# Performance work log

Hardware: AMD Instinct MI355X
Metric: run time of the kernel (lower is better)

The kernel has to match this reference:

```python
import jax, jax.numpy as jnp
import numpy as np

N, E, IN, H = 20000, 50000, 32, 64


def _lin_init(k, fan_in, shape):
    b = 1.0 / np.sqrt(fan_in)
    return jax.random.uniform(k, shape, jnp.float32, -b, b)


def setup_inputs() -> dict:
    key = jax.random.key(0)
    ks = jax.random.split(key, 16)
    inp = {
        "x": jax.random.normal(ks[0], (N, IN), jnp.float32),
        "edge_index": jax.random.randint(ks[1], (2, E), 0, N, dtype=jnp.int32),
        "edge_attr": jax.random.normal(ks[2], (E, 1, 2), jnp.float32),
        # layer 0: edge MLP 2->H->IN*H, root [IN,H], bias [H]
        "w1_0": _lin_init(ks[3], 2, (2, H)),
        "b1_0": _lin_init(ks[4], 2, (H,)),
        "w2_0": _lin_init(ks[5], H, (H, IN * H)),
        "b2_0": _lin_init(ks[6], H, (IN * H,)),
        "root_0": _lin_init(ks[7], IN, (IN, H)),
        "bias_0": _lin_init(ks[8], IN, (H,)),
        # layer 1: edge MLP 2->H->H*H, root [H,H], bias [H]
        "w1_1": _lin_init(ks[9], 2, (2, H)),
        "b1_1": _lin_init(ks[10], 2, (H,)),
        "w2_1": _lin_init(ks[11], H, (H, H * H)),
        "b2_1": _lin_init(ks[12], H, (H * H,)),
        "root_1": _lin_init(ks[13], H, (H, H)),
        "bias_1": _lin_init(ks[14], H, (H,)),
    }
    return inp


def _nnconv(x, src, dst, ea, w1, b1, w2, b2, root, bias, in_c, out_c):
    # per-edge weight matrices from edge-attr MLP: [E, in_c*out_c]
    h = jax.nn.relu(ea @ w1 + b1) @ w2 + b2
    W = h.reshape(-1, in_c, out_c)                     # [E, in, out]
    msg = jnp.einsum('ei,eio->eo', x[src], W)          # gather + per-edge matmul
    agg = jax.ops.segment_sum(msg, dst, num_segments=x.shape[0])  # scatter-add
    return agg + x @ root + bias                       # add aggr (PyG NNConv, aggr='add')


def reference(x, edge_index, edge_attr,
              w1_0, b1_0, w2_0, b2_0, root_0, bias_0,
              w1_1, b1_1, w2_1, b2_1, root_1, bias_1):
    src, dst = edge_index[0], edge_index[1]
    ea = edge_attr.reshape(edge_attr.shape[0], 2)      # [E, 2]
    x = jax.nn.relu(_nnconv(x, src, dst, ea, w1_0, b1_0, w2_0, b2_0, root_0, bias_0, IN, H))
    x = jax.nn.relu(_nnconv(x, src, dst, ea, w1_1, b1_1, w2_1, b2_1, root_1, bias_1, H, H))
    return x
```

## Files before the change

kernel.cpp:

```cpp
#include <hip/hip_runtime.h>

typedef _Float16 v8h __attribute__((ext_vector_type(8)));
typedef float v16f __attribute__((ext_vector_type(16)));

__global__ void prep_fused(const float* __restrict__ w2_0, const float* __restrict__ b2_0,
                           _Float16* __restrict__ BF0,
                           const float* __restrict__ w2_1, const float* __restrict__ b2_1,
                           _Float16* __restrict__ BF1,
                           const float* __restrict__ x, const float* __restrict__ root,
                           const float* __restrict__ bias, float* __restrict__ agg,
                           _Float16* __restrict__ xb, int N) {
    int idx = blockIdx.x * 256 + threadIdx.x;
    const int n0 = 264 * 512;
    const int n1 = 528 * 512;
    if (idx < n0 + n1) {
        const float* w2; const float* b2; _Float16* BF; int IN, rel;
        if (idx < n0) { w2 = w2_0; b2 = b2_0; BF = BF0; IN = 32; rel = idx; }
        else          { w2 = w2_1; b2 = b2_1; BF = BF1; IN = 64; rel = idx - n0; }
        int j = rel & 7, lane = (rel >> 3) & 63, f = rel >> 9;
        int nf = f & 1, kk16 = f >> 1;
        int ln = lane & 31, g2 = lane >> 5;
        int k = kk16 * 16 + g2 * 8 + j;
        int ko = k / IN, i = k - ko * IN;
        int o = nf * 32 + ln;
        float v = (ko < 64) ? w2[ko * (IN * 64) + i * 64 + o]
                : (ko == 64 ? b2[i * 64 + o] : 0.f);
        BF[rel] = (_Float16)v;
        return;
    }
    idx -= (n0 + n1);
    if (idx >= N * 64) return;
    int n = idx >> 6, o = idx & 63;
    float s = bias[o];
    const float* xr = x + (size_t)n * 32;
    #pragma unroll 8
    for (int i = 0; i < 32; ++i) s += xr[i] * root[i * 64 + o];
    agg[idx] = s;
    if (o < 32) xb[n * 32 + o] = (_Float16)xr[o];
}

__global__ void mid_kernel(const float* __restrict__ agg0, const float* __restrict__ root1,
                           const float* __restrict__ bias1, _Float16* __restrict__ x1b,
                           float* __restrict__ agg1, int N) {
    int idx = blockIdx.x * 256 + threadIdx.x;
    if (idx >= N * 64) return;
    int n = idx >> 6, o = idx & 63;
    const float* ar = agg0 + (size_t)n * 64;
    float s = bias1[o];
    #pragma unroll 8
    for (int i = 0; i < 64; ++i) s += fmaxf(ar[i], 0.f) * root1[i * 64 + o];
    agg1[idx] = s;
    x1b[idx] = (_Float16)fmaxf(agg0[idx], 0.f);
}

__global__ void final_relu(const float* __restrict__ agg1, float* __restrict__ out, int n) {
    int idx = blockIdx.x * 256 + threadIdx.x;
    if (idx < n) out[idx] = fmaxf(agg1[idx], 0.f);
}

template<int IN_C>
__global__ __launch_bounds__(256, 2)
void edge_gemm(const float* __restrict__ ea,
               const float* __restrict__ w1, const float* __restrict__ b1,
               const _Float16* __restrict__ xb, const _Float16* __restrict__ BF,
               const int* __restrict__ srcI, const int* __restrict__ dstI,
               float* __restrict__ agg, int E) {
    constexpr int PH  = IN_C / 16;
    constexpr int CPR = IN_C / 8;

    __shared__ __align__(16) _Float16 sh_x[128][IN_C];
    __shared__ _Float16 sh_r1[128][66];
    __shared__ float buf[128][65];
    __shared__ int sh_dst[128];

    int tid = threadIdx.x;
    int ebase = blockIdx.x * 128;
    int valid = E - ebase; if (valid > 128) valid = 128;

    if (tid < 128) {
        sh_dst[tid] = (tid < valid) ? dstI[ebase + tid] : 0;
        sh_r1[tid][64] = (_Float16)1.f;
        sh_r1[tid][65] = (_Float16)0.f;
    }
    for (int i = tid; i < 128 * 64; i += 256) {
        int e = i >> 6, j = i & 63;
        int ge = (e < valid) ? (ebase + e) : ebase;
        float a0 = ea[ge * 2], a1 = ea[ge * 2 + 1];
        sh_r1[e][j] = (_Float16)fmaxf(a0 * w1[j] + a1 * w1[64 + j] + b1[j], 0.f);
    }
    for (int i = tid; i < 128 * CPR; i += 256) {
        int r = i / CPR, c = i - r * CPR;
        int sidx = (r < valid) ? srcI[ebase + r] : 0;
        *(uint4*)&sh_x[r][c * 8] = *(const uint4*)(xb + (size_t)sidx * IN_C + (size_t)c * 8);
    }
    __syncthreads();

    int wv = tid >> 6, lane = tid & 63, ln = lane & 31, g2 = lane >> 5;
    int nf = wv & 1, kh = wv >> 1;

    v8h xs0[PH], xs1[PH], xs2[PH], xs3[PH];
    #pragma unroll
    for (int p = 0; p < PH; ++p) {
        xs0[p] = *(const v8h*)&sh_x[ln     ][p * 16 + g2 * 8];
        xs1[p] = *(const v8h*)&sh_x[ln + 32][p * 16 + g2 * 8];
        xs2[p] = *(const v8h*)&sh_x[ln + 64][p * 16 + g2 * 8];
        xs3[p] = *(const v8h*)&sh_x[ln + 96][p * 16 + g2 * 8];
    }

    v16f acc0 = {0,0,0,0,0,0,0,0,0,0,0,0,0,0,0,0};
    v16f acc1 = acc0, acc2 = acc0, acc3 = acc0;

    const uint4* bp = (const uint4*)BF + (size_t)nf * 64 + lane;
    int kb = kh * 33;

    uint4 b[PH], bn[PH];
    auto LD = [&](uint4 (&d)[PH], int ko) {
        #pragma unroll
        for (int p = 0; p < PH; ++p) d[p] = bp[(size_t)(ko * PH + p) * 128];
    };
    auto FM = [&](uint4 (&d)[PH], int ko) {
        _Float16 sv0 = sh_r1[ln     ][ko];
        _Float16 sv1 = sh_r1[ln + 32][ko];
        _Float16 sv2 = sh_r1[ln + 64][ko];
        _Float16 sv3 = sh_r1[ln + 96][ko];
        #pragma unroll
        for (int p = 0; p < PH; ++p) {
            v8h bb; __builtin_memcpy(&bb, &d[p], 16);
            acc0 = __builtin_amdgcn_mfma_f32_32x32x16_f16(xs0[p] * sv0, bb, acc0, 0, 0, 0);
            acc1 = __builtin_amdgcn_mfma_f32_32x32x16_f16(xs1[p] * sv1, bb, acc1, 0, 0, 0);
            acc2 = __builtin_amdgcn_mfma_f32_32x32x16_f16(xs2[p] * sv2, bb, acc2, 0, 0, 0);
            acc3 = __builtin_amdgcn_mfma_f32_32x32x16_f16(xs3[p] * sv3, bb, acc3, 0, 0, 0);
        }
    };

    LD(b, kb);
    #pragma unroll 1
    for (int t = 0; t < 16; ++t) {
        LD(bn, kb + 2 * t + 1);
        FM(b,  kb + 2 * t);
        LD(b,  kb + 2 * t + 2);
        FM(bn, kb + 2 * t + 1);
    }
    FM(b, kb + 32);

    int colb = nf * 32 + ln;
    if (kh == 1) {
        #pragma unroll
        for (int r = 0; r < 16; ++r) {
            int row = 4 * g2 + (r & 3) + 8 * (r >> 2);
            buf[row     ][colb] = acc0[r];
            buf[row + 32][colb] = acc1[r];
            buf[row + 64][colb] = acc2[r];
            buf[row + 96][colb] = acc3[r];
        }
    }
    __syncthreads();
    if (kh == 0) {
        #pragma unroll
        for (int r = 0; r < 16; ++r) {
            int row = 4 * g2 + (r & 3) + 8 * (r >> 2);
            if (row < valid)
                atomicAdd(&agg[(size_t)sh_dst[row] * 64 + colb], acc0[r] + buf[row][colb]);
            int row1 = row + 32;
            if (row1 < valid)
                atomicAdd(&agg[(size_t)sh_dst[row1] * 64 + colb], acc1[r] + buf[row1][colb]);
            int row2 = row + 64;
            if (row2 < valid)
                atomicAdd(&agg[(size_t)sh_dst[row2] * 64 + colb], acc2[r] + buf[row2][colb]);
            int row3 = row + 96;
            if (row3 < valid)
                atomicAdd(&agg[(size_t)sh_dst[row3] * 64 + colb], acc3[r] + buf[row3][colb]);
        }
    }
}

extern "C" void kernel_launch(void* const* d_in, const int* in_sizes, int n_in,
                              void* d_out, int out_size, void* d_ws, size_t ws_size,
                              hipStream_t stream) {
    const float* x      = (const float*)d_in[0];
    const int*   ei     = (const int*)d_in[1];
    const float* ea     = (const float*)d_in[2];
    const float* w1_0   = (const float*)d_in[3];
    const float* b1_0   = (const float*)d_in[4];
    const float* w2_0   = (const float*)d_in[5];
    const float* b2_0   = (const float*)d_in[6];
    const float* root_0 = (const float*)d_in[7];
    const float* bias_0 = (const float*)d_in[8];
    const float* w1_1   = (const float*)d_in[9];
    const float* b1_1   = (const float*)d_in[10];
    const float* w2_1   = (const float*)d_in[11];
    const float* b2_1   = (const float*)d_in[12];
    const float* root_1 = (const float*)d_in[13];
    const float* bias_1 = (const float*)d_in[14];
    float* out = (float*)d_out;

    int N = in_sizes[0] / 32;
    int E = in_sizes[1] / 2;
    const int* srcI = ei;
    const int* dstI = ei + E;

    char* ws = (char*)d_ws;
    size_t off = 0;
    auto carve = [&](size_t bytes) {
        void* p = ws + off;
        off += (bytes + 255) & ~(size_t)255;
        return p;
    };
    _Float16* BF0  = (_Float16*)carve((size_t)264 * 512 * 2);
    _Float16* BF1  = (_Float16*)carve((size_t)528 * 512 * 2);
    _Float16* XB0  = (_Float16*)carve((size_t)N * 32 * 2);
    _Float16* X1B  = (_Float16*)carve((size_t)N * 64 * 2);
    float*    AGG0 = (float*)carve((size_t)N * 64 * 4);
    float*    AGG1 = (float*)carve((size_t)N * 64 * 4);

    int tprep = (264 + 528) * 512 + N * 64;
    prep_fused<<<(tprep + 255) / 256, 256, 0, stream>>>(w2_0, b2_0, BF0, w2_1, b2_1, BF1,
                                                        x, root_0, bias_0, AGG0, XB0, N);

    int gblocks = (E + 127) / 128;
    edge_gemm<32><<<gblocks, 256, 0, stream>>>(ea, w1_0, b1_0, XB0, BF0, srcI, dstI, AGG0, E);

    mid_kernel<<<(N * 64 + 255) / 256, 256, 0, stream>>>(AGG0, root_1, bias_1, X1B, AGG1, N);

    edge_gemm<64><<<gblocks, 256, 0, stream>>>(ea, w1_1, b1_1, X1B, BF1, srcI, dstI, AGG1, E);

    final_relu<<<(N * 64 + 255) / 256, 256, 0, stream>>>(AGG1, out, N * 64);
}
```

Measured before the change: 183.7 us.

## Shrink edge tile to 96 rows, alias LDS buffers, triple-buffer B loads

Cuts the per-block edge tile from 128 to 96 rows, which removes one accumulator set and its x fragments. The x/r1 staging LDS is aliased with the reduction buffer, guarded by an extra barrier, which lowers LDS and register use per block and should allow more resident blocks. The K loop moves from double- to triple-buffered B-fragment loads, with the r1 scale values prefetched alongside them. In exchange each B fragment is reused across fewer rows, so more blocks re-read the weights, and the extra barrier adds a sync.

```diff
diff --git a/kernel.cpp b/kernel.cpp
--- a/kernel.cpp
+++ b/kernel.cpp
@@ -67,28 +67,35 @@
                float* __restrict__ agg, int E) {
     constexpr int PH  = IN_C / 16;
     constexpr int CPR = IN_C / 8;
-
-    __shared__ __align__(16) _Float16 sh_x[128][IN_C];
-    __shared__ _Float16 sh_r1[128][66];
-    __shared__ float buf[128][65];
-    __shared__ int sh_dst[128];
+    constexpr int M   = 96;
+
+    constexpr size_t XBYTES = (size_t)M * IN_C * 2;
+    constexpr size_t RBYTES = (size_t)M * 66 * 2;
+    constexpr size_t BBYTES = (size_t)M * 65 * 4;
+    constexpr size_t SBYTES = (XBYTES + RBYTES > BBYTES) ? (XBYTES + RBYTES) : BBYTES;
+
+    __shared__ __align__(16) char smem[SBYTES];
+    __shared__ int sh_dst[M];
+    auto sh_x  = (_Float16 (*)[IN_C])smem;
+    auto sh_r1 = (_Float16 (*)[66])(smem + XBYTES);
+    auto buf   = (float (*)[65])smem;
 
     int tid = threadIdx.x;
-    int ebase = blockIdx.x * 128;
-    int valid = E - ebase; if (valid > 128) valid = 128;
-
-    if (tid < 128) {
+    int ebase = blockIdx.x * M;
+    int valid = E - ebase; if (valid > M) valid = M;
+
+    if (tid < M) {
         sh_dst[tid] = (tid < valid) ? dstI[ebase + tid] : 0;
         sh_r1[tid][64] = (_Float16)1.f;
         sh_r1[tid][65] = (_Float16)0.f;
     }
-    for (int i = tid; i < 128 * 64; i += 256) {
+    for (int i = tid; i < M * 64; i += 256) {
         int e = i >> 6, j = i & 63;
         int ge = (e < valid) ? (ebase + e) : ebase;
-        float a0 = ea[ge * 2], a1 = ea[ge * 2 + 1];
-        sh_r1[e][j] = (_Float16)fmaxf(a0 * w1[j] + a1 * w1[64 + j] + b1[j], 0.f);
-    }
-    for (int i = tid; i < 128 * CPR; i += 256) {
+        float2 av = *(const float2*)(ea + (size_t)ge * 2);
+        sh_r1[e][j] = (_Float16)fmaxf(av.x * w1[j] + av.y * w1[64 + j] + b1[j], 0.f);
+    }
+    for (int i = tid; i < M * CPR; i += 256) {
         int r = i / CPR, c = i - r * CPR;
         int sidx = (r < valid) ? srcI[ebase + r] : 0;
         *(uint4*)&sh_x[r][c * 8] = *(const uint4*)(xb + (size_t)sidx * IN_C + (size_t)c * 8);
@@ -98,52 +105,55 @@
     int wv = tid >> 6, lane = tid & 63, ln = lane & 31, g2 = lane >> 5;
     int nf = wv & 1, kh = wv >> 1;
 
-    v8h xs0[PH], xs1[PH], xs2[PH], xs3[PH];
+    v8h xs0[PH], xs1[PH], xs2[PH];
     #pragma unroll
     for (int p = 0; p < PH; ++p) {
         xs0[p] = *(const v8h*)&sh_x[ln     ][p * 16 + g2 * 8];
         xs1[p] = *(const v8h*)&sh_x[ln + 32][p * 16 + g2 * 8];
         xs2[p] = *(const v8h*)&sh_x[ln + 64][p * 16 + g2 * 8];
-        xs3[p] = *(const v8h*)&sh_x[ln + 96][p * 16 + g2 * 8];
     }
 
     v16f acc0 = {0,0,0,0,0,0,0,0,0,0,0,0,0,0,0,0};
-    v16f acc1 = acc0, acc2 = acc0, acc3 = acc0;
+    v16f acc1 = acc0, acc2 = acc0;
 
     const uint4* bp = (const uint4*)BF + (size_t)nf * 64 + lane;
     int kb = kh * 33;
 
-    uint4 b[PH], bn[PH];
+    uint4 b0[PH], b1v[PH], b2v[PH];
+    _Float16 s0[3], s1[3], s2[3];
+
     auto LD = [&](uint4 (&d)[PH], int ko) {
         #pragma unroll
         for (int p = 0; p < PH; ++p) d[p] = bp[(size_t)(ko * PH + p) * 128];
     };
-    auto FM = [&](uint4 (&d)[PH], int ko) {
-        _Float16 sv0 = sh_r1[ln     ][ko];
-        _Float16 sv1 = sh_r1[ln + 32][ko];
-        _Float16 sv2 = sh_r1[ln + 64][ko];
-        _Float16 sv3 = sh_r1[ln + 96][ko];
+    auto SV = [&](_Float16 (&s)[3], int ko) {
+        s[0] = sh_r1[ln     ][ko];
+        s[1] = sh_r1[ln + 32][ko];
+        s[2] = sh_r1[ln + 64][ko];
+    };
+    auto FM = [&](uint4 (&d)[PH], _Float16 (&s)[3]) {
         #pragma unroll
         for (int p = 0; p < PH; ++p) {
             v8h bb; __builtin_memcpy(&bb, &d[p], 16);
-            acc0 = __builtin_amdgcn_mfma_f32_32x32x16_f16(xs0[p] * sv0, bb, acc0, 0, 0, 0);
-            acc1 = __builtin_amdgcn_mfma_f32_32x32x16_f16(xs1[p] * sv1, bb, acc1, 0, 0, 0);
-            acc2 = __builtin_amdgcn_mfma_f32_32x32x16_f16(xs2[p] * sv2, bb, acc2, 0, 0, 0);
-            acc3 = __builtin_amdgcn_mfma_f32_32x32x16_f16(xs3[p] * sv3, bb, acc3, 0, 0, 0);
+            acc0 = __builtin_amdgcn_mfma_f32_32x32x16_f16(xs0[p] * s[0], bb, acc0, 0, 0, 0);
+            acc1 = __builtin_amdgcn_mfma_f32_32x32x16_f16(xs1[p] * s[1], bb, acc1, 0, 0, 0);
+            acc2 = __builtin_amdgcn_mfma_f32_32x32x16_f16(xs2[p] * s[2], bb, acc2, 0, 0, 0);
         }
     };
 
-    LD(b, kb);
+    LD(b0, kb);     SV(s0, kb);
+    LD(b1v, kb + 1); SV(s1, kb + 1);
     #pragma unroll 1
-    for (int t = 0; t < 16; ++t) {
-        LD(bn, kb + 2 * t + 1);
-        FM(b,  kb + 2 * t);
-        LD(b,  kb + 2 * t + 2);
-        FM(bn, kb + 2 * t + 1);
-    }
-    FM(b, kb + 32);
+    for (int t = 0; t < 30; t += 3) {
+        LD(b2v, kb + t + 2); SV(s2, kb + t + 2); FM(b0,  s0);
+        LD(b0,  kb + t + 3); SV(s0, kb + t + 3); FM(b1v, s1);
+        LD(b1v, kb + t + 4); SV(s1, kb + t + 4); FM(b2v, s2);
+    }
+    LD(b2v, kb + 32); SV(s2, kb + 32);
+    FM(b0, s0); FM(b1v, s1); FM(b2v, s2);
 
     int colb = nf * 32 + ln;
+    __syncthreads();
     if (kh == 1) {
         #pragma unroll
         for (int r = 0; r < 16; ++r) {
@@ -151,7 +161,6 @@
             buf[row     ][colb] = acc0[r];
             buf[row + 32][colb] = acc1[r];
             buf[row + 64][colb] = acc2[r];
-            buf[row + 96][colb] = acc3[r];
         }
     }
     __syncthreads();
@@ -167,9 +176,6 @@
             int row2 = row + 64;
             if (row2 < valid)
                 atomicAdd(&agg[(size_t)sh_dst[row2] * 64 + colb], acc2[r] + buf[row2][colb]);
-            int row3 = row + 96;
-            if (row3 < valid)
-                atomicAdd(&agg[(size_t)sh_dst[row3] * 64 + colb], acc3[r] + buf[row3][colb]);
         }
     }
 }
@@ -217,7 +223,7 @@
     prep_fused<<<(tprep + 255) / 256, 256, 0, stream>>>(w2_0, b2_0, BF0, w2_1, b2_1, BF1,
                                                         x, root_0, bias_0, AGG0, XB0, N);
 
-    int gblocks = (E + 127) / 128;
+    int gblocks = (E + 95) / 96;
     edge_gemm<32><<<gblocks, 256, 0, stream>>>(ea, w1_0, b1_0, XB0, BF0, srcI, dstI, AGG0, E);
 
     mid_kernel<<<(N * 64 + 255) / 256, 256, 0, stream>>>(AGG0, root_1, bias_1, X1B, AGG1, N);
```

New measurement: 198.6 us. 1.08x slower.

## Double edge tile to 256 per block with 8 waves sharing weight loads

Applied to the files above, without the earlier changes.

The edge GEMM block now covers 256 edges with 512 threads. Two groups of four waves each take one 128-edge half, and the waves in the same position across the halves read the same weight fragments at the same time, which should raise L2 reuse of the BF weight stream and halve the block count. Shared memory is overlapped: the reduction buffer aliases the x/r1 staging area, which requires an extra barrier. The edge-attribute load is also vectorised to float2. In exchange, fewer blocks (196) may give less occupancy and load balance across the GPU's CUs.

```diff
diff --git a/kernel.cpp b/kernel.cpp
--- a/kernel.cpp
+++ b/kernel.cpp
@@ -59,7 +59,7 @@
 }
 
 template<int IN_C>
-__global__ __launch_bounds__(256, 2)
+__global__ __launch_bounds__(512, 2)
 void edge_gemm(const float* __restrict__ ea,
                const float* __restrict__ w1, const float* __restrict__ b1,
                const _Float16* __restrict__ xb, const _Float16* __restrict__ BF,
@@ -67,28 +67,35 @@
                float* __restrict__ agg, int E) {
     constexpr int PH  = IN_C / 16;
     constexpr int CPR = IN_C / 8;
-
-    __shared__ __align__(16) _Float16 sh_x[128][IN_C];
-    __shared__ _Float16 sh_r1[128][66];
-    __shared__ float buf[128][65];
-    __shared__ int sh_dst[128];
+    constexpr int M   = 256;
+
+    constexpr size_t XBYTES = (size_t)M * IN_C * 2;
+    constexpr size_t RBYTES = (size_t)M * 66 * 2;
+    constexpr size_t BBYTES = (size_t)M * 65 * 4;
+    constexpr size_t SBYTES = (XBYTES + RBYTES > BBYTES) ? (XBYTES + RBYTES) : BBYTES;
+
+    __shared__ __align__(16) char smem[SBYTES];
+    __shared__ int sh_dst[M];
+    auto sh_x  = (_Float16 (*)[IN_C])smem;
+    auto sh_r1 = (_Float16 (*)[66])(smem + XBYTES);
+    auto buf   = (float (*)[65])smem;
 
     int tid = threadIdx.x;
-    int ebase = blockIdx.x * 128;
-    int valid = E - ebase; if (valid > 128) valid = 128;
-
-    if (tid < 128) {
+    int ebase = blockIdx.x * M;
+    int valid = E - ebase; if (valid > M) valid = M;
+
+    if (tid < M) {
         sh_dst[tid] = (tid < valid) ? dstI[ebase + tid] : 0;
         sh_r1[tid][64] = (_Float16)1.f;
         sh_r1[tid][65] = (_Float16)0.f;
     }
-    for (int i = tid; i < 128 * 64; i += 256) {
+    for (int i = tid; i < M * 64; i += 512) {
         int e = i >> 6, j = i & 63;
         int ge = (e < valid) ? (ebase + e) : ebase;
-        float a0 = ea[ge * 2], a1 = ea[ge * 2 + 1];
-        sh_r1[e][j] = (_Float16)fmaxf(a0 * w1[j] + a1 * w1[64 + j] + b1[j], 0.f);
-    }
-    for (int i = tid; i < 128 * CPR; i += 256) {
+        float2 av = *(const float2*)(ea + (size_t)ge * 2);
+        sh_r1[e][j] = (_Float16)fmaxf(av.x * w1[j] + av.y * w1[64 + j] + b1[j], 0.f);
+    }
+    for (int i = tid; i < M * CPR; i += 512) {
         int r = i / CPR, c = i - r * CPR;
         int sidx = (r < valid) ? srcI[ebase + r] : 0;
         *(uint4*)&sh_x[r][c * 8] = *(const uint4*)(xb + (size_t)sidx * IN_C + (size_t)c * 8);
@@ -96,15 +103,16 @@
     __syncthreads();
 
     int wv = tid >> 6, lane = tid & 63, ln = lane & 31, g2 = lane >> 5;
-    int nf = wv & 1, kh = wv >> 1;
+    int nf = wv & 1, kh = (wv >> 1) & 1, mh = wv >> 2;
+    int mbase = mh * 128;
 
     v8h xs0[PH], xs1[PH], xs2[PH], xs3[PH];
     #pragma unroll
     for (int p = 0; p < PH; ++p) {
-        xs0[p] = *(const v8h*)&sh_x[ln     ][p * 16 + g2 * 8];
-        xs1[p] = *(const v8h*)&sh_x[ln + 32][p * 16 + g2 * 8];
-        xs2[p] = *(const v8h*)&sh_x[ln + 64][p * 16 + g2 * 8];
-        xs3[p] = *(const v8h*)&sh_x[ln + 96][p * 16 + g2 * 8];
+        xs0[p] = *(const v8h*)&sh_x[mbase + ln     ][p * 16 + g2 * 8];
+        xs1[p] = *(const v8h*)&sh_x[mbase + ln + 32][p * 16 + g2 * 8];
+        xs2[p] = *(const v8h*)&sh_x[mbase + ln + 64][p * 16 + g2 * 8];
+        xs3[p] = *(const v8h*)&sh_x[mbase + ln + 96][p * 16 + g2 * 8];
     }
 
     v16f acc0 = {0,0,0,0,0,0,0,0,0,0,0,0,0,0,0,0};
@@ -119,10 +127,10 @@
         for (int p = 0; p < PH; ++p) d[p] = bp[(size_t)(ko * PH + p) * 128];
     };
     auto FM = [&](uint4 (&d)[PH], int ko) {
-        _Float16 sv0 = sh_r1[ln     ][ko];
-        _Float16 sv1 = sh_r1[ln + 32][ko];
-        _Float16 sv2 = sh_r1[ln + 64][ko];
-        _Float16 sv3 = sh_r1[ln + 96][ko];
+        _Float16 sv0 = sh_r1[mbase + ln     ][ko];
+        _Float16 sv1 = sh_r1[mbase + ln + 32][ko];
+        _Float16 sv2 = sh_r1[mbase + ln + 64][ko];
+        _Float16 sv3 = sh_r1[mbase + ln + 96][ko];
         #pragma unroll
         for (int p = 0; p < PH; ++p) {
             v8h bb; __builtin_memcpy(&bb, &d[p], 16);
@@ -144,10 +152,11 @@
     FM(b, kb + 32);
 
     int colb = nf * 32 + ln;
+    __syncthreads();
     if (kh == 1) {
         #pragma unroll
         for (int r = 0; r < 16; ++r) {
-            int row = 4 * g2 + (r & 3) + 8 * (r >> 2);
+            int row = mbase + 4 * g2 + (r & 3) + 8 * (r >> 2);
             buf[row     ][colb] = acc0[r];
             buf[row + 32][colb] = acc1[r];
             buf[row + 64][colb] = acc2[r];
@@ -158,7 +167,7 @@
     if (kh == 0) {
         #pragma unroll
         for (int r = 0; r < 16; ++r) {
-            int row = 4 * g2 + (r & 3) + 8 * (r >> 2);
+            int row = mbase + 4 * g2 + (r & 3) + 8 * (r >> 2);
             if (row < valid)
                 atomicAdd(&agg[(size_t)sh_dst[row] * 64 + colb], acc0[r] + buf[row][colb]);
             int row1 = row + 32;
@@ -217,12 +226,12 @@
     prep_fused<<<(tprep + 255) / 256, 256, 0, stream>>>(w2_0, b2_0, BF0, w2_1, b2_1, BF1,
                                                         x, root_0, bias_0, AGG0, XB0, N);
 
-    int gblocks = (E + 127) / 128;
-    edge_gemm<32><<<gblocks, 256, 0, stream>>>(ea, w1_0, b1_0, XB0, BF0, srcI, dstI, AGG0, E);
+    int gblocks = (E + 255) / 256;
+    edge_gemm<32><<<gblocks, 512, 0, stream>>>(ea, w1_0, b1_0, XB0, BF0, srcI, dstI, AGG0, E);
 
     mid_kernel<<<(N * 64 + 255) / 256, 256, 0, stream>>>(AGG0, root_1, bias_1, X1B, AGG1, N);
 
-    edge_gemm<64><<<gblocks, 256, 0, stream>>>(ea, w1_1, b1_1, X1B, BF1, srcI, dstI, AGG1, E);
+    edge_gemm<64><<<gblocks, 512, 0, stream>>>(ea, w1_1, b1_1, X1B, BF1, srcI, dstI, AGG1, E);
 
     final_relu<<<(N * 64 + 255) / 256, 256, 0, stream>>>(AGG1, out, N * 64);
 }
```

New measurement: 193.2 us. 5.1% more time.
